# Performance work log

Hardware: AMD Instinct MI355X
Metric: run time of the kernel (lower is better)

## Reference

```python
import jax, jax.numpy as jnp
import numpy as np

K = 15; P = 3; IN_CH = 128; OUT_CH = 128
NQ_LRF = 4; NS_LRF = 4; LRF_CH = IN_CH // NQ_LRF  # 32
KP_EXTENT = 1.2; RADIUS = 2.5
NQ = 10000; NS = 10000; H = 32


def setup_inputs() -> dict:
    key = jax.random.key(0)
    ks = jax.random.split(key, 10)
    return {
        "q_pts": jax.random.normal(ks[0], (NQ, P), jnp.float32),
        "s_pts": jax.random.normal(ks[1], (NS, P), jnp.float32),
        "neighb_inds": jax.random.randint(ks[2], (NQ, H), 0, NS + 1),  # index NS == shadow point
        "x": jax.random.normal(ks[3], (NS, IN_CH), jnp.float32),
        "q_lrf": jax.random.normal(ks[4], (NQ, NQ_LRF, P, P), jnp.float32),
        "s_lrf": jax.random.normal(ks[5], (NS, NS_LRF, P, P), jnp.float32),
        "weights": jax.random.normal(ks[6], (K, 2 * IN_CH, OUT_CH), jnp.float32) * 0.02,
        "kernel_points": jax.random.normal(ks[7], (K, P), jnp.float32) * (RADIUS * 0.3),
        "mlp_w": jax.random.normal(ks[8], (NS_LRF * P * P, LRF_CH), jnp.float32) * 0.1,
        "mlp_b": jnp.zeros((LRF_CH,), jnp.float32),
    }


def _forward(q_pts, s_pts, neighb_inds, x, q_lrf, s_lrf, weights, kernel_points, mlp_w, mlp_b):
    Nq, Hn = neighb_inds.shape
    Ns = s_pts.shape[0]
    # q_lrf is only ever used detached in the torch module; kernel points are non-trainable
    q_lrf_d = jax.lax.stop_gradient(q_lrf)
    kp = jax.lax.stop_gradient(kernel_points)

    # gather neighbor coords (shadow row at +1e6), center on queries
    s_pts_pad = jnp.concatenate([s_pts, jnp.full((1, P), 1e6, s_pts.dtype)], 0)
    neighbors = s_pts_pad[neighb_inds] - q_pts[:, None, :]            # [Nq,H,3]
    # rotate into each query LRF
    aligned = jnp.einsum('nhd,nqde->nqhe', neighbors, q_lrf_d)        # [Nq,nq,H,3]
    sq_d = jnp.sum((aligned[..., None, :] - kp) ** 2, axis=-1)        # [Nq,nq,H,K]

    # aligned neighbor LRFs: q_lrf^T @ s_lrf_neighbor
    s_lrf_pad = jnp.concatenate([s_lrf, jnp.zeros_like(s_lrf[:1])], 0)
    nb_lrf = s_lrf_pad[neighb_inds]                                   # [Nq,H,ns,3,3]
    aligned_lrf = jnp.einsum('nqba,nhsbc->nhqsac', q_lrf_d, nb_lrf)   # [Nq,H,nq,ns,3,3]
    aligned_lrf = aligned_lrf.reshape(Nq, Hn, NQ_LRF, NS_LRF * P * P)
    lrf_feat = aligned_lrf @ mlp_w + mlp_b                            # [Nq,H,nq,lrf_ch]
    mask = (neighb_inds < Ns).astype(lrf_feat.dtype)                  # shadow-neighbor mask
    lrf_feat = lrf_feat * mask[:, :, None, None]

    # linear kernel-point influence
    all_w = jnp.clip(1.0 - jnp.sqrt(sq_d) / KP_EXTENT, 0.0)           # [Nq,nq,H,K]
    all_w = jnp.swapaxes(all_w, 2, 3)                                 # [Nq,nq,K,H]

    # gather neighbor features (zero shadow row), append lrf features
    x_pad = jnp.concatenate([x.reshape(Ns, NQ_LRF, LRF_CH),
                             jnp.zeros((1, NQ_LRF, LRF_CH), x.dtype)], 0)
    nb_x = x_pad[neighb_inds]                                         # [Nq,H,nq,lc]
    nb_x = jnp.concatenate([nb_x, lrf_feat], axis=-1)                 # [Nq,H,nq,2lc]
    nb_x = jnp.swapaxes(nb_x, 1, 2)                                   # [Nq,nq,H,2lc]

    # influence-weighted aggregation over neighbors, then per-kernel matmul
    wf = jnp.matmul(all_w, nb_x)                                      # [Nq,nq,K,2lc]
    wf = jnp.transpose(wf, (2, 0, 1, 3)).reshape(K, Nq, 2 * IN_CH)    # [K,Nq,fdim]
    return jnp.einsum('knf,kfo->no', wf, weights)                     # [Nq,out]


def reference(q_pts, s_pts, neighb_inds, x, q_lrf, s_lrf, weights, kernel_points, mlp_w, mlp_b):
    return _forward(q_pts, s_pts, neighb_inds, x, q_lrf, s_lrf, weights, kernel_points, mlp_w, mlp_b)
```

## Files before the change

### kernel.cpp

```cpp
#include <hip/hip_runtime.h>

#define NQn 10000
#define NSn 10000
#define Hh  32
#define FDIM 3840

typedef _Float16 f16x8 __attribute__((ext_vector_type(8)));
typedef float    f32x4 __attribute__((ext_vector_type(4)));

__device__ __forceinline__ unsigned pack2h(float a, float b) {
  union { _Float16 h; unsigned short u; } ua, ub;
  ua.h = (_Float16)a; ub.h = (_Float16)b;
  return (unsigned)ua.u | ((unsigned)ub.u << 16);
}

__global__ __launch_bounds__(256) void ekp_prep5(
    const float* __restrict__ w, const float* __restrict__ x,
    _Float16* __restrict__ wt, _Float16* __restrict__ xh)
{
  const int b = blockIdx.x, tid = threadIdx.x;
  if (b < 625) {
    size_t base = (size_t)b*2048 + (size_t)tid*8;
    float4 a0 = *reinterpret_cast<const float4*>(x + base);
    float4 a1 = *reinterpret_cast<const float4*>(x + base + 4);
    uint4 o;
    o.x = pack2h(a0.x, a0.y); o.y = pack2h(a0.z, a0.w);
    o.z = pack2h(a1.x, a1.y); o.w = pack2h(a1.z, a1.w);
    *reinterpret_cast<uint4*>(xh + base) = o;
  } else if (b == 625) {
    if (tid < 64)
      reinterpret_cast<unsigned*>(xh + (size_t)NSn*128)[tid] = 0u;
  } else {
    __shared__ _Float16 t[32][34];
    const int tt = b - 626;
    const int k0 = (tt % 120) * 32, n0 = (tt / 120) * 32;
    const int c = tid & 31, r0 = tid >> 5;
    #pragma unroll
    for (int p = 0; p < 4; ++p) {
      int r = r0 + p*8;
      t[c][r] = (_Float16)w[(size_t)(k0 + r)*128 + n0 + c];
    }
    __syncthreads();
    #pragma unroll
    for (int p = 0; p < 4; ++p) {
      int r = r0 + p*8;
      wt[(size_t)(n0 + r)*FDIM + k0 + c] = t[r][c];
    }
  }
}

__global__ __launch_bounds__(256, 4) void ekp_stage1h(
    const float* __restrict__ q_pts, const float* __restrict__ s_pts,
    const int*   __restrict__ nbi,   const unsigned short* __restrict__ xh,
    const float* __restrict__ q_lrf, const float* __restrict__ s_lrf,
    const float* __restrict__ kp,    const float* __restrict__ mlp_w,
    const float* __restrict__ mlp_b, _Float16* __restrict__ wf_out)
{
  const int n = blockIdx.x;
  const int tid = threadIdx.x;
  const int lane = tid & 63;
  const int wv = tid >> 6;
  const int l15 = lane & 15, lg = lane >> 4;

  __shared__ float sQ[36];
  __shared__ float sMB[32];
  __shared__ int   sIdx[32];
  __shared__ int   sIdxX[32];
  __shared__ float sZ[32];
  __shared__ float sNbr[32][3];
  __shared__ alignas(16) _Float16 sLrfA[32][72];
  __shared__ alignas(16) _Float16 sBw2[4][32][72];
  __shared__ alignas(16) _Float16 sWb[4][16][40];
  __shared__ alignas(16) _Float16 sFt[4][32][40];

  if (tid < 36) sQ[tid]  = q_lrf[(size_t)n*36 + tid];
  if (tid < 32) sMB[tid] = mlp_b[tid];
  if (tid < 32) {
    int idx = nbi[(size_t)n*Hh + tid];
    int sh = (idx >= NSn) ? 1 : 0;
    sZ[tid]    = sh ? 0.f : 1.f;
    sIdx[tid]  = sh ? 0 : idx;
    sIdxX[tid] = idx;
  }
  { unsigned* z = (unsigned*)&sBw2[0][0][0];
    for (int i = tid; i < 4608; i += 256) z[i] = 0u; }
  { unsigned* z = (unsigned*)&sLrfA[0][0];
    for (int i = tid; i < 1152; i += 256) z[i] = 0u; }
  __syncthreads();

  if (tid < 96) {
    int h = tid / 3, d = tid - h*3;
    sNbr[h][d] = sZ[h] * s_pts[(size_t)sIdx[h]*3 + d] - q_pts[(size_t)n*3 + d];
  }
  for (int f4i = tid; f4i < 288; f4i += 256) {
    int row = f4i / 9, c4 = f4i - row*9;
    float4 v = *reinterpret_cast<const float4*>(
        s_lrf + (size_t)sIdx[row]*36 + c4*4);
    float z = sZ[row];
    uint2 pk;
    pk.x = pack2h(z*v.x, z*v.y);
    pk.y = pack2h(z*v.z, z*v.w);
    *reinterpret_cast<uint2*>(&sLrfA[row][c4*4]) = pk;
  }
  #pragma unroll
  for (int it = 0; it < 18; ++it) {
    int i = tid + it*256;
    int q = i / 1152, r = i - q*1152;
    int k = r >> 5, m = r & 31;
    int s = k / 9, bc = k - s*9, b = bc / 3, c = bc - b*3;
    int br = (s*9 + c)*32 + m;
    float acc = sQ[q*9 + b*3 + 0] * mlp_w[br]
              + sQ[q*9 + b*3 + 1] * mlp_w[br + 96]
              + sQ[q*9 + b*3 + 2] * mlp_w[br + 192];
    sBw2[q][m][k] = (_Float16)acc;
  }
  __syncthreads();

  {
    int h = lane & 31, kh = lane >> 5;
    float a0 = 0.f, a1 = 0.f, a2 = 0.f;
    #pragma unroll
    for (int d = 0; d < 3; ++d) {
      float nd = sNbr[h][d];
      a0 += nd * sQ[wv*9 + d*3 + 0];
      a1 += nd * sQ[wv*9 + d*3 + 1];
      a2 += nd * sQ[wv*9 + d*3 + 2];
    }
    float z = sZ[h];
    int k0 = kh * 8, kend = kh ? 15 : 8;
    for (int k = k0; k < kend; ++k) {
      float d0 = a0 - kp[k*3+0];
      float d1 = a1 - kp[k*3+1];
      float d2 = a2 - kp[k*3+2];
      float wgt = 1.f - sqrtf(d0*d0 + d1*d1 + d2*d2) * (1.0f/1.2f);
      sWb[wv][k][h] = (_Float16)(z * fmaxf(wgt, 0.f));
    }
    if (kh) sWb[wv][15][h] = (_Float16)0.f;
  }
  {
    f32x4 fa[2][2];
    #pragma unroll
    for (int i = 0; i < 2; ++i)
      #pragma unroll
      for (int j = 0; j < 2; ++j) fa[i][j] = (f32x4){0.f,0.f,0.f,0.f};
    #pragma unroll
    for (int kc = 0; kc < 2; ++kc) {
      f16x8 af0 = *reinterpret_cast<const f16x8*>(&sLrfA[l15][kc*32 + lg*8]);
      f16x8 af1 = *reinterpret_cast<const f16x8*>(&sLrfA[16 + l15][kc*32 + lg*8]);
      f16x8 bf0 = *reinterpret_cast<const f16x8*>(&sBw2[wv][l15][kc*32 + lg*8]);
      f16x8 bf1 = *reinterpret_cast<const f16x8*>(&sBw2[wv][16 + l15][kc*32 + lg*8]);
      fa[0][0] = __builtin_amdgcn_mfma_f32_16x16x32_f16(af0, bf0, fa[0][0], 0, 0, 0);
      fa[0][1] = __builtin_amdgcn_mfma_f32_16x16x32_f16(af0, bf1, fa[0][1], 0, 0, 0);
      fa[1][0] = __builtin_amdgcn_mfma_f32_16x16x32_f16(af1, bf0, fa[1][0], 0, 0, 0);
      fa[1][1] = __builtin_amdgcn_mfma_f32_16x16x32_f16(af1, bf1, fa[1][1], 0, 0, 0);
    }
    #pragma unroll
    for (int ht = 0; ht < 2; ++ht) {
      int hb = ht*16 + lg*4;
      float z0 = sZ[hb+0], z1 = sZ[hb+1], z2 = sZ[hb+2], z3 = sZ[hb+3];
      #pragma unroll
      for (int mt = 0; mt < 2; ++mt) {
        int m = mt*16 + l15;
        float bias = sMB[m];
        uint2 pk;
        pk.x = pack2h(fmaf(z0, bias, fa[ht][mt][0]), fmaf(z1, bias, fa[ht][mt][1]));
        pk.y = pack2h(fmaf(z2, bias, fa[ht][mt][2]), fmaf(z3, bias, fa[ht][mt][3]));
        *reinterpret_cast<uint2*>(&sFt[wv][m][hb]) = pk;
      }
    }
  }
  __syncthreads();

  {
    f16x8 a = *reinterpret_cast<const f16x8*>(&sWb[wv][l15][lg*8]);
    union { unsigned u[4]; f16x8 v; } B0, B1;
    #pragma unroll
    for (int j = 0; j < 8; j += 2) {
      int h0 = lg*8 + j, h1 = h0 + 1;
      size_t r0 = (size_t)sIdxX[h0]*128 + wv*32 + l15;
      size_t r1 = (size_t)sIdxX[h1]*128 + wv*32 + l15;
      B0.u[j >> 1] = (unsigned)xh[r0]      | ((unsigned)xh[r1]      << 16);
      B1.u[j >> 1] = (unsigned)xh[r0 + 16] | ((unsigned)xh[r1 + 16] << 16);
    }
    f16x8 b2 = *reinterpret_cast<const f16x8*>(&sFt[wv][l15][lg*8]);
    f16x8 b3 = *reinterpret_cast<const f16x8*>(&sFt[wv][16 + l15][lg*8]);

    _Float16* wp = wf_out + (size_t)n*FDIM + wv*64 + l15;
    f32x4 acc;
    acc = (f32x4){0.f,0.f,0.f,0.f};
    acc = __builtin_amdgcn_mfma_f32_16x16x32_f16(a, B0.v, acc, 0, 0, 0);
    #pragma unroll
    for (int v = 0; v < 4; ++v) { int k = lg*4 + v; if (k < 15) wp[k*256 +  0] = (_Float16)acc[v]; }
    acc = (f32x4){0.f,0.f,0.f,0.f};
    acc = __builtin_amdgcn_mfma_f32_16x16x32_f16(a, B1.v, acc, 0, 0, 0);
    #pragma unroll
    for (int v = 0; v < 4; ++v) { int k = lg*4 + v; if (k < 15) wp[k*256 + 16] = (_Float16)acc[v]; }
    acc = (f32x4){0.f,0.f,0.f,0.f};
    acc = __builtin_amdgcn_mfma_f32_16x16x32_f16(a, b2, acc, 0, 0, 0);
    #pragma unroll
    for (int v = 0; v < 4; ++v) { int k = lg*4 + v; if (k < 15) wp[k*256 + 32] = (_Float16)acc[v]; }
    acc = (f32x4){0.f,0.f,0.f,0.f};
    acc = __builtin_amdgcn_mfma_f32_16x16x32_f16(a, b3, acc, 0, 0, 0);
    #pragma unroll
    for (int v = 0; v < 4; ++v) { int k = lg*4 + v; if (k < 15) wp[k*256 + 48] = (_Float16)acc[v]; }
  }
}

__global__ __launch_bounds__(256, 4) void ekp_gemm3(
    const _Float16* __restrict__ A,
    const _Float16* __restrict__ Bt,
    float* __restrict__ C)
{
  __shared__ alignas(16) _Float16 As[32][72];
  __shared__ alignas(16) _Float16 Bs[128][72];
  const int tid = threadIdx.x, lane = tid & 63, w = tid >> 6;
  const int wr = w >> 1, wc = w & 1;
  const int r0 = blockIdx.x * 32;
  const int l15 = lane & 15, lg = lane >> 4;

  f32x4 acc[4];
  #pragma unroll
  for (int i = 0; i < 4; ++i) acc[i] = (f32x4){0.f,0.f,0.f,0.f};

  const int sr = tid >> 3;
  const int ak = (tid & 7) << 3;
  const _Float16* ap = A  + (size_t)(r0 + sr)*FDIM + ak;
  const _Float16* bp = Bt + (size_t)sr*FDIM + ak;

  for (int kc = 0; kc < FDIM; kc += 64) {
    *reinterpret_cast<f16x8*>(&As[sr][ak]) = *reinterpret_cast<const f16x8*>(ap + kc);
    #pragma unroll
    for (int p = 0; p < 4; ++p)
      *reinterpret_cast<f16x8*>(&Bs[p*32 + sr][ak]) =
        *reinterpret_cast<const f16x8*>(bp + (size_t)p*32*FDIM + kc);
    __syncthreads();
    #pragma unroll
    for (int k2 = 0; k2 < 2; ++k2) {
      const int ko = k2*32 + lg*8;
      f16x8 a = *reinterpret_cast<const f16x8*>(&As[wr*16 + l15][ko]);
      #pragma unroll
      for (int ni = 0; ni < 4; ++ni) {
        f16x8 b = *reinterpret_cast<const f16x8*>(&Bs[wc*64 + ni*16 + l15][ko]);
        acc[ni] = __builtin_amdgcn_mfma_f32_16x16x32_f16(a, b, acc[ni], 0, 0, 0);
      }
    }
    __syncthreads();
  }
  #pragma unroll
  for (int v = 0; v < 4; ++v) {
    int gr = r0 + wr*16 + lg*4 + v;
    if (gr < NQn) {
      #pragma unroll
      for (int ni = 0; ni < 4; ++ni)
        C[(size_t)gr*128 + wc*64 + ni*16 + l15] = acc[ni][v];
    }
  }
}

__global__ __launch_bounds__(256) void ekp_stage1_fused(
    const float* __restrict__ q_pts, const float* __restrict__ s_pts,
    const int*   __restrict__ nbi,   const float* __restrict__ x,
    const float* __restrict__ q_lrf, const float* __restrict__ s_lrf,
    const float* __restrict__ weights, const float* __restrict__ kp,
    const float* __restrict__ mlp_w, const float* __restrict__ mlp_b,
    float* __restrict__ out)
{
  const int n = blockIdx.x;
  const int tid = threadIdx.x;

  __shared__ float sQ[36];
  __shared__ float sKP[45];
  __shared__ float sMW[36][32];
  __shared__ float sMB[32];
  __shared__ int   sIdx[32];
  __shared__ int   sShad[32];
  __shared__ float sNbr[32][3];
  __shared__ float sLrf[32][37];
  __shared__ float sW[4][15][32];
  __shared__ float sNbx[32][4][65];

  if (tid < 36) sQ[tid]  = q_lrf[(size_t)n*36 + tid];
  if (tid < 45) sKP[tid] = kp[tid];
  if (tid < 32) sMB[tid] = mlp_b[tid];
  for (int i = tid; i < 36*32; i += 256) sMW[i >> 5][i & 31] = mlp_w[i];
  if (tid < 32) {
    int idx = nbi[(size_t)n*Hh + tid];
    int sh = (idx >= NSn) ? 1 : 0;
    sShad[tid] = sh;
    sIdx[tid]  = sh ? 0 : idx;
  }
  __syncthreads();

  if (tid < 96) {
    int h = tid / 3, d = tid - h*3;
    float v = sShad[h] ? 0.f : s_pts[(size_t)sIdx[h]*3 + d];
    sNbr[h][d] = v - q_pts[(size_t)n*3 + d];
  }
  {
    int h = tid >> 3, j0 = tid & 7;
    const float* src = s_lrf + (size_t)sIdx[h]*36;
    float z = sShad[h] ? 0.f : 1.f;
    for (int j = j0; j < 36; j += 8) sLrf[h][j] = z * src[j];
  }
  for (int i = tid; i < Hh*128; i += 256) {
    int h = i >> 7, c = i & 127;
    float v = sShad[h] ? 0.f : x[(size_t)sIdx[h]*128 + c];
    sNbx[h][c >> 5][c & 31] = v;
  }
  __syncthreads();

  {
    int q = tid >> 6, l = tid & 63;
    int h = l & 31, kh = l >> 5;
    float a0 = 0.f, a1 = 0.f, a2 = 0.f;
    #pragma unroll
    for (int d = 0; d < 3; ++d) {
      float nd = sNbr[h][d];
      a0 += nd * sQ[q*9 + d*3 + 0];
      a1 += nd * sQ[q*9 + d*3 + 1];
      a2 += nd * sQ[q*9 + d*3 + 2];
    }
    float z = sShad[h] ? 0.f : 1.f;
    int k0 = kh * 8;
    int kend = k0 + (kh ? 7 : 8);
    for (int k = k0; k < kend; ++k) {
      float d0 = a0 - sKP[k*3+0];
      float d1 = a1 - sKP[k*3+1];
      float d2 = a2 - sKP[k*3+2];
      float wv2 = 1.f - sqrtf(d0*d0 + d1*d1 + d2*d2) * (1.0f/1.2f);
      sW[q][k][h] = z * fmaxf(wv2, 0.f);
    }
  }
  {
    int q = tid >> 6, l = tid & 63;
    int h = l & 31, mh = l >> 5;
    float fi[36];
    #pragma unroll
    for (int s = 0; s < 4; ++s)
      #pragma unroll
      for (int a = 0; a < 3; ++a)
        #pragma unroll
        for (int c = 0; c < 3; ++c) {
          float accv = 0.f;
          #pragma unroll
          for (int b = 0; b < 3; ++b)
            accv += sQ[q*9 + b*3 + a] * sLrf[h][s*9 + b*3 + c];
          fi[s*9 + a*3 + c] = accv;
        }
    float z = sShad[h] ? 0.f : 1.f;
    int m0 = mh * 16;
    for (int mm = 0; mm < 16; ++mm) {
      int m = m0 + mm;
      float accv = sMB[m];
      #pragma unroll
      for (int j = 0; j < 36; ++j) accv += fi[j] * sMW[j][m];
      sNbx[h][q][32 + m] = z * accv;
    }
  }
  __syncthreads();

  float acc[15];
  const int q = tid >> 6, cch = tid & 63;
  #pragma unroll
  for (int k = 0; k < 15; ++k) acc[k] = 0.f;
  for (int h = 0; h < Hh; ++h) {
    float v = sNbx[h][q][cch];
    #pragma unroll
    for (int k = 0; k < 15; ++k) acc[k] += sW[q][k][h] * v;
  }

  __shared__ float sWF[FDIM];
  __shared__ float sRed[2][128];
  #pragma unroll
  for (int k = 0; k < 15; ++k) sWF[k*256 + q*64 + cch] = acc[k];
  __syncthreads();
  int o = tid & 127, part = tid >> 7;
  const float* wp = weights + (size_t)part*1920*128 + o;
  const float* wfp = sWF + part*1920;
  float oa = 0.f;
  #pragma unroll 8
  for (int f = 0; f < 1920; ++f)
    oa += wfp[f] * wp[(size_t)f*128];
  sRed[part][o] = oa;
  __syncthreads();
  if (tid < 128) out[(size_t)n*128 + tid] = sRed[0][tid] + sRed[1][tid];
}

extern "C" void kernel_launch(void* const* d_in, const int* in_sizes, int n_in,
                              void* d_out, int out_size, void* d_ws, size_t ws_size,
                              hipStream_t stream) {
  const float* q_pts   = (const float*)d_in[0];
  const float* s_pts   = (const float*)d_in[1];
  const int*   nbi     = (const int*)  d_in[2];
  const float* x       = (const float*)d_in[3];
  const float* q_lrf   = (const float*)d_in[4];
  const float* s_lrf   = (const float*)d_in[5];
  const float* weights = (const float*)d_in[6];
  const float* kp      = (const float*)d_in[7];
  const float* mlp_w   = (const float*)d_in[8];
  const float* mlp_b   = (const float*)d_in[9];
  float* out = (float*)d_out;

  const size_t nWf = (size_t)NQn * FDIM;
  const size_t nWt = (size_t)128 * FDIM;
  const size_t nXh = (size_t)(NSn + 1) * 128;
  const size_t needBytes = (nWf + nWt + nXh) * sizeof(_Float16);
  if (ws_size >= needBytes) {
    _Float16* wf = (_Float16*)d_ws;
    _Float16* wt = wf + nWf;
    _Float16* xh = wt + nWt;
    ekp_prep5<<<1106, 256, 0, stream>>>(weights, x, wt, xh);
    ekp_stage1h<<<NQn, 256, 0, stream>>>(q_pts, s_pts, nbi,
                                         (const unsigned short*)xh,
                                         q_lrf, s_lrf, kp, mlp_w, mlp_b, wf);
    ekp_gemm3<<<(NQn + 31)/32, 256, 0, stream>>>(wf, wt, out);
  } else {
    ekp_stage1_fused<<<NQn, 256, 0, stream>>>(q_pts, s_pts, nbi, x, q_lrf, s_lrf,
                                              weights, kp, mlp_w, mlp_b, out);
  }
}
```

Measured before the change: 144.0 us.

## Reorder intermediate feature layout to kernel-minor padded 4096 for vectorized stores

Changes the wf intermediate layout from k-major strided (k*256 + col) to col-major with 16 kernel slots per column, padding FDIM from 3840 to 4096 and zeroing the 16th kernel slot in the transposed weights. Stage1 can now write each MFMA result as one packed 8-byte store instead of four scattered 2-byte stores. The cost is about 6.7% more bytes for the intermediate and the weights, and extra K iterations in the GEMM that multiply by zero padding.

After: 146.2 us. No clear change (+1.5%).

```diff
diff --git a/kernel.cpp b/kernel.cpp
--- a/kernel.cpp
+++ b/kernel.cpp
@@ -3,7 +3,8 @@
 #define NQn 10000
 #define NSn 10000
 #define Hh  32
-#define FDIM 3840
+#define FDIM  3840
+#define FDIMP 4096
 
 typedef _Float16 f16x8 __attribute__((ext_vector_type(8)));
 typedef float    f32x4 __attribute__((ext_vector_type(4)));
@@ -14,7 +15,7 @@
   return (unsigned)ua.u | ((unsigned)ub.u << 16);
 }
 
-__global__ __launch_bounds__(256) void ekp_prep5(
+__global__ __launch_bounds__(256) void ekp_prep6(
     const float* __restrict__ w, const float* __restrict__ x,
     _Float16* __restrict__ wt, _Float16* __restrict__ xh)
 {
@@ -33,23 +34,28 @@
   } else {
     __shared__ _Float16 t[32][34];
     const int tt = b - 626;
-    const int k0 = (tt % 120) * 32, n0 = (tt / 120) * 32;
+    const int f0 = (tt & 127) * 32;
+    const int o0 = (tt >> 7) * 32;
     const int c = tid & 31, r0 = tid >> 5;
     #pragma unroll
     for (int p = 0; p < 4; ++p) {
       int r = r0 + p*8;
-      t[c][r] = (_Float16)w[(size_t)(k0 + r)*128 + n0 + c];
+      int f = f0 + r;
+      int k = f & 15, col = f >> 4;
+      t[c][r] = (k < 15)
+        ? (_Float16)w[(size_t)(k*256 + col)*128 + o0 + c]
+        : (_Float16)0.f;
     }
     __syncthreads();
     #pragma unroll
     for (int p = 0; p < 4; ++p) {
       int r = r0 + p*8;
-      wt[(size_t)(n0 + r)*FDIM + k0 + c] = t[r][c];
-    }
-  }
-}
-
-__global__ __launch_bounds__(256, 4) void ekp_stage1h(
+      wt[(size_t)(o0 + r)*FDIMP + f0 + c] = t[r][c];
+    }
+  }
+}
+
+__global__ __launch_bounds__(256, 4) void ekp_stage1i(
     const float* __restrict__ q_pts, const float* __restrict__ s_pts,
     const int*   __restrict__ nbi,   const unsigned short* __restrict__ xh,
     const float* __restrict__ q_lrf, const float* __restrict__ s_lrf,
@@ -185,28 +191,28 @@
     f16x8 b2 = *reinterpret_cast<const f16x8*>(&sFt[wv][l15][lg*8]);
     f16x8 b3 = *reinterpret_cast<const f16x8*>(&sFt[wv][16 + l15][lg*8]);
 
-    _Float16* wp = wf_out + (size_t)n*FDIM + wv*64 + l15;
-    f32x4 acc;
+    _Float16* wp = wf_out + (size_t)n*FDIMP + ((wv*64 + l15) << 4) + (lg << 2);
+    f32x4 acc;  uint2 pk;
     acc = (f32x4){0.f,0.f,0.f,0.f};
     acc = __builtin_amdgcn_mfma_f32_16x16x32_f16(a, B0.v, acc, 0, 0, 0);
-    #pragma unroll
-    for (int v = 0; v < 4; ++v) { int k = lg*4 + v; if (k < 15) wp[k*256 +  0] = (_Float16)acc[v]; }
+    pk.x = pack2h(acc[0], acc[1]); pk.y = pack2h(acc[2], acc[3]);
+    *reinterpret_cast<uint2*>(wp) = pk;
     acc = (f32x4){0.f,0.f,0.f,0.f};
     acc = __builtin_amdgcn_mfma_f32_16x16x32_f16(a, B1.v, acc, 0, 0, 0);
-    #pragma unroll
-    for (int v = 0; v < 4; ++v) { int k = lg*4 + v; if (k < 15) wp[k*256 + 16] = (_Float16)acc[v]; }
+    pk.x = pack2h(acc[0], acc[1]); pk.y = pack2h(acc[2], acc[3]);
+    *reinterpret_cast<uint2*>(wp + 256) = pk;
     acc = (f32x4){0.f,0.f,0.f,0.f};
     acc = __builtin_amdgcn_mfma_f32_16x16x32_f16(a, b2, acc, 0, 0, 0);
-    #pragma unroll
-    for (int v = 0; v < 4; ++v) { int k = lg*4 + v; if (k < 15) wp[k*256 + 32] = (_Float16)acc[v]; }
+    pk.x = pack2h(acc[0], acc[1]); pk.y = pack2h(acc[2], acc[3]);
+    *reinterpret_cast<uint2*>(wp + 512) = pk;
     acc = (f32x4){0.f,0.f,0.f,0.f};
     acc = __builtin_amdgcn_mfma_f32_16x16x32_f16(a, b3, acc, 0, 0, 0);
-    #pragma unroll
-    for (int v = 0; v < 4; ++v) { int k = lg*4 + v; if (k < 15) wp[k*256 + 48] = (_Float16)acc[v]; }
-  }
-}
-
-__global__ __launch_bounds__(256, 4) void ekp_gemm3(
+    pk.x = pack2h(acc[0], acc[1]); pk.y = pack2h(acc[2], acc[3]);
+    *reinterpret_cast<uint2*>(wp + 768) = pk;
+  }
+}
+
+__global__ __launch_bounds__(256, 4) void ekp_gemm4(
     const _Float16* __restrict__ A,
     const _Float16* __restrict__ Bt,
     float* __restrict__ C)
@@ -224,15 +230,15 @@
 
   const int sr = tid >> 3;
   const int ak = (tid & 7) << 3;
-  const _Float16* ap = A  + (size_t)(r0 + sr)*FDIM + ak;
-  const _Float16* bp = Bt + (size_t)sr*FDIM + ak;
-
-  for (int kc = 0; kc < FDIM; kc += 64) {
+  const _Float16* ap = A  + (size_t)(r0 + sr)*FDIMP + ak;
+  const _Float16* bp = Bt + (size_t)sr*FDIMP + ak;
+
+  for (int kc = 0; kc < FDIMP; kc += 64) {
     *reinterpret_cast<f16x8*>(&As[sr][ak]) = *reinterpret_cast<const f16x8*>(ap + kc);
     #pragma unroll
     for (int p = 0; p < 4; ++p)
       *reinterpret_cast<f16x8*>(&Bs[p*32 + sr][ak]) =
-        *reinterpret_cast<const f16x8*>(bp + (size_t)p*32*FDIM + kc);
+        *reinterpret_cast<const f16x8*>(bp + (size_t)p*32*FDIMP + kc);
     __syncthreads();
     #pragma unroll
     for (int k2 = 0; k2 < 2; ++k2) {
@@ -401,19 +407,19 @@
   const float* mlp_b   = (const float*)d_in[9];
   float* out = (float*)d_out;
 
-  const size_t nWf = (size_t)NQn * FDIM;
-  const size_t nWt = (size_t)128 * FDIM;
+  const size_t nWf = (size_t)NQn * FDIMP;
+  const size_t nWt = (size_t)128 * FDIMP;
   const size_t nXh = (size_t)(NSn + 1) * 128;
   const size_t needBytes = (nWf + nWt + nXh) * sizeof(_Float16);
   if (ws_size >= needBytes) {
     _Float16* wf = (_Float16*)d_ws;
     _Float16* wt = wf + nWf;
     _Float16* xh = wt + nWt;
-    ekp_prep5<<<1106, 256, 0, stream>>>(weights, x, wt, xh);
-    ekp_stage1h<<<NQn, 256, 0, stream>>>(q_pts, s_pts, nbi,
+    ekp_prep6<<<1138, 256, 0, stream>>>(weights, x, wt, xh);
+    ekp_stage1i<<<NQn, 256, 0, stream>>>(q_pts, s_pts, nbi,
                                          (const unsigned short*)xh,
                                          q_lrf, s_lrf, kp, mlp_w, mlp_b, wf);
-    ekp_gemm3<<<(NQn + 31)/32, 256, 0, stream>>>(wf, wt, out);
+    ekp_gemm4<<<(NQn + 31)/32, 256, 0, stream>>>(wf, wt, out);
   } else {
     ekp_stage1_fused<<<NQn, 256, 0, stream>>>(q_pts, s_pts, nbi, x, q_lrf, s_lrf,
                                               weights, kp, mlp_w, mlp_b, out);
```
